# Optimization experiments

Hardware: AMD Instinct MI355X
Metric: run time of the kernel (lower is better)

## Reference

```python
import jax, jax.numpy as jnp
import numpy as np

WS = 7  # window_size
HEADS = 12
HEAD_DIM = 32
HIDDEN = 384
INNER = HEADS * HEAD_DIM


def _relative_position_index(ws):
    coords = np.stack(np.meshgrid(np.arange(ws), np.arange(ws), indexing='ij'))  # (2, ws, ws)
    flat = coords.reshape(2, -1)  # (2, ws*ws)
    rel = flat[:, :, None] - flat[:, None, :]  # (2, N, N)
    rel = rel.transpose(1, 2, 0).copy()
    rel[:, :, 0] += ws - 1
    rel[:, :, 1] += ws - 1
    rel[:, :, 0] *= 2 * ws - 1
    return rel.sum(-1)  # (N, N) int


def setup_inputs() -> dict:
    key = jax.random.key(0)
    k1, k2, k3, k4, k5 = jax.random.split(key, 5)
    x = jax.random.normal(k1, (32, 56, 56, HIDDEN), dtype=jnp.float32)
    w_qkv = jax.random.normal(k2, (HIDDEN, INNER * 3), dtype=jnp.float32) * (HIDDEN ** -0.5)
    w_out = jax.random.normal(k3, (INNER, HIDDEN), dtype=jnp.float32) * (INNER ** -0.5)
    b_out = jax.random.normal(k4, (HIDDEN,), dtype=jnp.float32) * 0.02
    bias_table = jax.random.normal(k5, ((2 * WS - 1) * (2 * WS - 1), HEADS), dtype=jnp.float32) * 0.02
    return {"x": x, "w_qkv": w_qkv, "w_out": w_out, "b_out": b_out, "bias_table": bias_table}


def _window_attention(x, w_qkv, w_out, b_out, bias_table):
    b, n_h, n_w, _ = x.shape
    ws, h, d = WS, HEADS, HEAD_DIM
    nw_h, nw_w = n_h // ws, n_w // ws
    N = ws * ws

    qkv = x @ w_qkv  # (b, n_h, n_w, 3*inner)
    q, k, v = jnp.split(qkv, 3, axis=-1)

    def to_windows(t):
        # (b, n_h, n_w, h*d) -> (b, h, nw_h*nw_w, ws*ws, d)
        t = t.reshape(b, nw_h, ws, nw_w, ws, h, d)
        t = t.transpose(0, 5, 1, 3, 2, 4, 6)
        return t.reshape(b, h, nw_h * nw_w, N, d)

    q, k, v = map(to_windows, (q, k, v))
    scale = d ** -0.5
    dots = jnp.einsum('bhwid,bhwjd->bhwij', q, k) * scale
    attn = jax.nn.softmax(dots, axis=-1)

    rel_idx = jnp.asarray(_relative_position_index(ws))  # (N, N)
    bias = bias_table[rel_idx.reshape(-1)].reshape(N, N, h)  # gather
    bias = bias.transpose(2, 0, 1)  # (h, N, N)
    # NOTE: faithful to source — bias added AFTER softmax
    attn = attn + bias[None, :, None, :, :]

    out = jnp.einsum('bhwij,bhwjd->bhwid', attn, v)  # (b, h, nw, N, d)
    out = out.reshape(b, h, nw_h, nw_w, ws, ws, d)
    out = out.transpose(0, 2, 4, 3, 5, 1, 6).reshape(b, n_h, n_w, h * d)
    return out @ w_out + b_out


def reference(x, w_qkv, w_out, b_out, bias_table):
    return _window_attention(x, w_qkv, w_out, b_out, bias_table)
```

## Files before the change

### kernel.cpp

```cpp
#include <hip/hip_runtime.h>
#include <hip/hip_bf16.h>
#include <cstdint>

#define TOK 100352
#define HID 384
#define NQKV 1152
#define NHEADS 12
#define HDIM 32

typedef __attribute__((ext_vector_type(8))) short bhalf8;
typedef __attribute__((ext_vector_type(4))) float f32x4;

__device__ __forceinline__ ushort f2bf(float f) {
  uint32_t u = __float_as_uint(f);
  return (ushort)((u + 0x7FFFu + ((u >> 16) & 1u)) >> 16);
}

__device__ __forceinline__ void gload_lds16(const ushort* g, ushort* l) {
  __builtin_amdgcn_global_load_lds(
      (const __attribute__((address_space(1))) unsigned int*)g,
      (__attribute__((address_space(3))) unsigned int*)l, 16, 0, 0);
}

__device__ __forceinline__ uint32_t cvtpk(float a, float b) {
  uint32_t r;
  asm("v_cvt_pk_bf16_f32 %0, %1, %2" : "=v"(r) : "v"(a), "v"(b));
  return r;
}

__global__ __launch_bounds__(256)
void cvt_bf16(const float* __restrict__ in, ushort* __restrict__ out, const int n8) {
  const int i = blockIdx.x * 256 + threadIdx.x;
  if (i >= n8) return;
  const float4 f0 = ((const float4*)in)[(size_t)i * 2];
  const float4 f1 = ((const float4*)in)[(size_t)i * 2 + 1];
  bhalf8 v;
  v[0] = (short)f2bf(f0.x); v[1] = (short)f2bf(f0.y);
  v[2] = (short)f2bf(f0.z); v[3] = (short)f2bf(f0.w);
  v[4] = (short)f2bf(f1.x); v[5] = (short)f2bf(f1.y);
  v[6] = (short)f2bf(f1.z); v[7] = (short)f2bf(f1.w);
  ((bhalf8*)out)[i] = v;
}

__global__ __launch_bounds__(256)
void transpose_cvt(const float* __restrict__ in, ushort* __restrict__ out,
                   const int R, const int C) {
  const int i = blockIdx.x * 256 + threadIdx.x;
  if (i >= R * C) return;
  const int r = i % R, c = i / R;
  out[i] = f2bf(in[(size_t)r * C + c]);
}

__global__ __launch_bounds__(256)
void expand_bias_pad(const float* __restrict__ bt, float* __restrict__ bx) {
  const int i = blockIdx.x * 256 + threadIdx.x;
  if (i >= NHEADS * 49 * 64) return;
  const int head = i / (49 * 64);
  const int rem = i % (49 * 64);
  const int q = rem / 64, k = rem % 64;
  float v = 0.f;
  if (k < 49) {
    const int idx = (q / 7 - k / 7 + 6) * 13 + (q % 7 - k % 7 + 6);
    v = bt[idx * NHEADS + head];
  }
  bx[i] = v;
}

template<bool OUT_F32_BIAS>
__global__ __launch_bounds__(256)
void gemm_bt(const ushort* __restrict__ A, const ushort* __restrict__ Bt,
             const float* __restrict__ bias, void* __restrict__ Cp,
             const int N, const int K, const int nbx, const int row_ofs)
{
  __shared__ ushort As[128 * 64];
  __shared__ ushort Bs[128 * 64];

  const int tid = threadIdx.x;
  const int lane = tid & 63;
  const int wave = tid >> 6;
  const int wm = wave >> 1, wn = wave & 1;
  const int l15 = lane & 15, l16 = lane >> 4;

  int bid = blockIdx.x;
  const int nwg = gridDim.x;
  if ((nwg & 7) == 0) bid = (bid & 7) * (nwg >> 3) + (bid >> 3);
  const int row0 = (bid / nbx) * 128 + row_ofs;
  const int col0 = (bid % nbx) * 128;

  f32x4 acc[4][4] = {};

  for (int ko = 0; ko < K; ko += 64) {
    if (ko) __syncthreads();
    #pragma unroll
    for (int it = 0; it < 4; ++it) {
      const int chunk = it * 4 + wave;
      const int idx = chunk * 64 + lane;
      const int m = idx >> 3;
      const int k8 = (((idx & 7) ^ (m & 7)) * 8);
      gload_lds16(A + (size_t)(row0 + m) * K + ko + k8, &As[chunk * 512]);
      gload_lds16(Bt + (size_t)(col0 + m) * K + ko + k8, &Bs[chunk * 512]);
    }
    __syncthreads();
    #pragma unroll
    for (int kk = 0; kk < 64; kk += 32) {
      bhalf8 af[4], bfr[4];
      #pragma unroll
      for (int f = 0; f < 4; ++f) {
        const int ra = wm * 64 + f * 16 + l15;
        const int rb = wn * 64 + f * 16 + l15;
        const int kb = (kk + l16 * 8) * 2;
        af[f]  = *(const bhalf8*)((const char*)As + ra * 128 + (kb ^ ((ra & 7) << 4)));
        bfr[f] = *(const bhalf8*)((const char*)Bs + rb * 128 + (kb ^ ((rb & 7) << 4)));
      }
      #pragma unroll
      for (int fm = 0; fm < 4; ++fm)
        #pragma unroll
        for (int fn = 0; fn < 4; ++fn)
          acc[fm][fn] = __builtin_amdgcn_mfma_f32_16x16x32_bf16(af[fm], bfr[fn], acc[fm][fn], 0, 0, 0);
    }
  }

  #pragma unroll
  for (int fm = 0; fm < 4; ++fm) {
    const int rb = row0 + wm * 64 + fm * 16 + l16 * 4;
    #pragma unroll
    for (int fn = 0; fn < 4; ++fn) {
      const int cc = col0 + wn * 64 + fn * 16 + l15;
      const float badd = OUT_F32_BIAS ? bias[cc] : 0.f;
      #pragma unroll
      for (int i = 0; i < 4; ++i) {
        const float vv = acc[fm][fn][i] + badd;
        if (OUT_F32_BIAS) ((float*)Cp)[(size_t)(rb + i) * N + cc] = vv;
        else ((ushort*)Cp)[(size_t)(rb + i) * N + cc] = f2bf(vv);
      }
    }
  }
}

__global__ __launch_bounds__(256)
void win_attn4(const ushort* __restrict__ qkv, const float* __restrict__ biasx,
               ushort* __restrict__ attn_out)
{
  __shared__ ushort VtAll[4][32 * 64];
  __shared__ ushort PsAll[4][64 * 64];

  const int tid = threadIdx.x;
  const int lane = tid & 63, wave = tid >> 6;
  const int l15 = lane & 15, l16 = lane >> 4;
  const int gid = blockIdx.x * 4 + wave;
  const int head = gid % NHEADS;
  const int win = gid / NHEADS;
  const int b = win >> 6, wi = (win >> 3) & 7, wj = win & 7;
  char* Vt = (char*)VtAll[wave];
  char* Ps = (char*)PsAll[wave];

  const int base_row = b * 3136 + wi * 7 * 56 + wj * 7;

  #pragma unroll
  for (int it = 0; it < 4; ++it) {
    const int t = lane;
    const int d0 = it * 8;
    bhalf8 v = {0, 0, 0, 0, 0, 0, 0, 0};
    if (t < 49) {
      const size_t off = (size_t)(base_row + (t / 7) * 56 + (t % 7)) * NQKV
                         + 768 + head * HDIM + d0;
      v = *(const bhalf8*)(qkv + off);
    }
    #pragma unroll
    for (int j = 0; j < 8; ++j) {
      const int d = d0 + j;
      const int byteoff = ((d * 64 + t) * 2) ^ ((d & 7) << 4);
      *(ushort*)(Vt + byteoff) = (ushort)v[j];
    }
  }

  bhalf8 qf[4], kf[4];
  #pragma unroll
  for (int f = 0; f < 4; ++f) {
    const int r = f * 16 + l15;
    const int rr = r < 49 ? r : 48;
    const size_t off = (size_t)(base_row + (rr / 7) * 56 + (rr % 7)) * NQKV
                       + head * HDIM + l16 * 8;
    qf[f] = *(const bhalf8*)(qkv + off);
    kf[f] = *(const bhalf8*)(qkv + off + 384);
  }

  const f32x4 fz = {};
  f32x4 s[4][4];
  #pragma unroll
  for (int fm = 0; fm < 4; ++fm)
    #pragma unroll
    for (int fn = 0; fn < 4; ++fn)
      s[fm][fn] = __builtin_amdgcn_mfma_f32_16x16x32_bf16(kf[fm], qf[fn], fz, 0, 0, 0);

  const float scale = 0.17677669529663687f;
  const float* bq = biasx + (size_t)head * (49 * 64);

  #pragma unroll
  for (int fn = 0; fn < 4; ++fn) {
    const int q = fn * 16 + l15;
    const int xr = (q & 7) << 4;
    char* prow = Ps + q * 128;
    if (fn == 3 && l15 != 0) {
      #pragma unroll
      for (int fm = 0; fm < 4; ++fm) {
        const int b0 = (fm * 16 + l16 * 4) * 2;
        *(uint32_t*)(prow + (b0 ^ xr)) = 0u;
        *(uint32_t*)(prow + (b0 ^ xr) + 4) = 0u;
      }
    } else {
      float e[4][4];
      float local = 0.f;
      #pragma unroll
      for (int fm = 0; fm < 3; ++fm)
        #pragma unroll
        for (int i = 0; i < 4; ++i) {
          e[fm][i] = __expf(s[fm][fn][i] * scale);
          local += e[fm][i];
        }
      e[3][0] = e[3][1] = e[3][2] = e[3][3] = 0.f;
      if (l16 == 0) {
        e[3][0] = __expf(s[3][fn][0] * scale);
        local += e[3][0];
      }
      float sum = local + __shfl_xor(local, 16);
      sum += __shfl_xor(sum, 32);
      const float inv = __builtin_amdgcn_rcpf(sum);
      const float* b4p = bq + q * 64;
      #pragma unroll
      for (int fm = 0; fm < 4; ++fm) {
        const int k0 = fm * 16 + l16 * 4;
        const float4 b4 = *(const float4*)(b4p + k0);
        const uint32_t w0 = cvtpk(fmaf(e[fm][0], inv, b4.x),
                                  fmaf(e[fm][1], inv, b4.y));
        const uint32_t w1 = cvtpk(fmaf(e[fm][2], inv, b4.z),
                                  fmaf(e[fm][3], inv, b4.w));
        const int b0 = (k0 * 2) ^ xr;
        *(uint32_t*)(prow + b0) = w0;
        *(uint32_t*)(prow + b0 + 4) = w1;
      }
    }
  }

  f32x4 o[4][2] = {};
  #pragma unroll
  for (int kk = 0; kk < 64; kk += 32) {
    bhalf8 pf[4], vf[2];
    #pragma unroll
    for (int f = 0; f < 4; ++f) {
      const int r = f * 16 + l15;
      pf[f] = *(const bhalf8*)(Ps + (((r * 64 + kk + l16 * 8) * 2) ^ ((r & 7) << 4)));
    }
    #pragma unroll
    for (int f = 0; f < 2; ++f) {
      const int d = f * 16 + l15;
      vf[f] = *(const bhalf8*)(Vt + (((d * 64 + kk + l16 * 8) * 2) ^ ((d & 7) << 4)));
    }
    #pragma unroll
    for (int fm = 0; fm < 4; ++fm)
      #pragma unroll
      for (int fn = 0; fn < 2; ++fn)
        o[fm][fn] = __builtin_amdgcn_mfma_f32_16x16x32_bf16(pf[fm], vf[fn], o[fm][fn], 0, 0, 0);
  }

  #pragma unroll
  for (int fm = 0; fm < 4; ++fm) {
    #pragma unroll
    for (int i = 0; i < 4; ++i) {
      const int r = fm * 16 + l16 * 4 + i;
      if (r < 49) {
        const int grow = base_row + (r / 7) * 56 + (r % 7);
        #pragma unroll
        for (int fn = 0; fn < 2; ++fn) {
          const int d = fn * 16 + l15;
          attn_out[(size_t)grow * HID + head * HDIM + d] = f2bf(o[fm][fn][i]);
        }
      }
    }
  }
}

extern "C" void kernel_launch(void* const* d_in, const int* in_sizes, int n_in,
                              void* d_out, int out_size, void* d_ws, size_t ws_size,
                              hipStream_t stream) {
  const float* x          = (const float*)d_in[0];
  const float* w_qkv      = (const float*)d_in[1];
  const float* w_out      = (const float*)d_in[2];
  const float* b_out      = (const float*)d_in[3];
  const float* bias_table = (const float*)d_in[4];
  float* out = (float*)d_out;

  ushort* xb     = (ushort*)d_ws;
  ushort* qkv    = xb + (size_t)TOK * HID;
  ushort* wqkvT  = qkv + (size_t)TOK * NQKV;
  ushort* woutT  = wqkvT + (size_t)NQKV * HID;
  float*  biasx  = (float*)(woutT + (size_t)HID * HID);
  ushort* attn_o = xb;

  {
    const int n8 = TOK * HID / 8;
    cvt_bf16<<<dim3((n8 + 255) / 256), dim3(256), 0, stream>>>(x, xb, n8);
    transpose_cvt<<<dim3(HID * NQKV / 256), dim3(256), 0, stream>>>(w_qkv, wqkvT, HID, NQKV);
    transpose_cvt<<<dim3(HID * HID / 256), dim3(256), 0, stream>>>(w_out, woutT, HID, HID);
    expand_bias_pad<<<dim3((NHEADS * 49 * 64 + 255) / 256), dim3(256), 0, stream>>>(
        bias_table, biasx);
  }

  const int halfM = TOK / 2;
  gemm_bt<false><<<dim3((NQKV / 128) * (halfM / 128)), dim3(256), 0, stream>>>(
      xb, wqkvT, nullptr, qkv, NQKV, HID, NQKV / 128, 0);
  gemm_bt<false><<<dim3((NQKV / 128) * (halfM / 128)), dim3(256), 0, stream>>>(
      xb, wqkvT, nullptr, qkv, NQKV, HID, NQKV / 128, halfM);

  win_attn4<<<dim3(2048 * NHEADS / 4), dim3(256), 0, stream>>>(qkv, biasx, attn_o);

  gemm_bt<true><<<dim3((HID / 128) * (TOK / 128)), dim3(256), 0, stream>>>(
      attn_o, woutT, b_out, out, HID, HID, HID / 128, 0);
}
```

Before: 344.5 us.

## Scatter QKV GEMM output into per-window, per-head contiguous layout

The QKV GEMM epilogue now writes each element directly into a window-major layout where every (window, head) owns contiguous Q, K and V slices of 49x32 bf16. The attention kernel can then read Q/K/V with simple contiguous offsets instead of strided gathers across image rows. The GEMM kernels are also specialized with compile-time N/K. The cost is a scattered 2-byte store pattern in the GEMM epilogue, with more index arithmetic per element and possibly poorly coalesced writes.

```diff
diff --git a/kernel.cpp b/kernel.cpp
--- a/kernel.cpp
+++ b/kernel.cpp
@@ -7,6 +7,7 @@
 #define NQKV 1152
 #define NHEADS 12
 #define HDIM 32
+#define WSLICE 1568
 
 typedef __attribute__((ext_vector_type(8))) short bhalf8;
 typedef __attribute__((ext_vector_type(4))) float f32x4;
@@ -66,11 +67,9 @@
   bx[i] = v;
 }
 
-template<bool OUT_F32_BIAS>
-__global__ __launch_bounds__(256)
-void gemm_bt(const ushort* __restrict__ A, const ushort* __restrict__ Bt,
-             const float* __restrict__ bias, void* __restrict__ Cp,
-             const int N, const int K, const int nbx, const int row_ofs)
+__global__ __launch_bounds__(256)
+void gemm_qkv_sc(const ushort* __restrict__ A, const ushort* __restrict__ Bt,
+                 ushort* __restrict__ qkvw, const int row_ofs)
 {
   __shared__ ushort As[128 * 64];
   __shared__ ushort Bs[128 * 64];
@@ -84,12 +83,12 @@
   int bid = blockIdx.x;
   const int nwg = gridDim.x;
   if ((nwg & 7) == 0) bid = (bid & 7) * (nwg >> 3) + (bid >> 3);
-  const int row0 = (bid / nbx) * 128 + row_ofs;
-  const int col0 = (bid % nbx) * 128;
+  const int row0 = (bid / 9) * 128 + row_ofs;
+  const int col0 = (bid % 9) * 128;
 
   f32x4 acc[4][4] = {};
 
-  for (int ko = 0; ko < K; ko += 64) {
+  for (int ko = 0; ko < HID; ko += 64) {
     if (ko) __syncthreads();
     #pragma unroll
     for (int it = 0; it < 4; ++it) {
@@ -97,8 +96,8 @@
       const int idx = chunk * 64 + lane;
       const int m = idx >> 3;
       const int k8 = (((idx & 7) ^ (m & 7)) * 8);
-      gload_lds16(A + (size_t)(row0 + m) * K + ko + k8, &As[chunk * 512]);
-      gload_lds16(Bt + (size_t)(col0 + m) * K + ko + k8, &Bs[chunk * 512]);
+      gload_lds16(A + (size_t)(row0 + m) * HID + ko + k8, &As[chunk * 512]);
+      gload_lds16(Bt + (size_t)(col0 + m) * HID + ko + k8, &Bs[chunk * 512]);
     }
     __syncthreads();
     #pragma unroll
@@ -122,23 +121,94 @@
 
   #pragma unroll
   for (int fm = 0; fm < 4; ++fm) {
+    #pragma unroll
+    for (int i = 0; i < 4; ++i) {
+      const int token = row0 + wm * 64 + fm * 16 + l16 * 4 + i;
+      const int bb = token / 3136, rem = token % 3136;
+      const int y = rem / 56, xx = rem % 56;
+      const int win = bb * 64 + (y / 7) * 8 + (xx / 7);
+      const int t = (y % 7) * 7 + (xx % 7);
+      ushort* tb = qkvw + (size_t)win * (NHEADS * 3 * WSLICE) + t * 32;
+      #pragma unroll
+      for (int fn = 0; fn < 4; ++fn) {
+        const int cc = col0 + wn * 64 + fn * 16 + l15;
+        const int sel = cc / 384;
+        const int hd = (cc % 384) >> 5;
+        const int d = cc & 31;
+        tb[(size_t)(hd * 3 + sel) * WSLICE + d] = f2bf(acc[fm][fn][i]);
+      }
+    }
+  }
+}
+
+__global__ __launch_bounds__(256)
+void gemm_out(const ushort* __restrict__ A, const ushort* __restrict__ Bt,
+              const float* __restrict__ bias, float* __restrict__ Cp)
+{
+  __shared__ ushort As[128 * 64];
+  __shared__ ushort Bs[128 * 64];
+
+  const int tid = threadIdx.x;
+  const int lane = tid & 63;
+  const int wave = tid >> 6;
+  const int wm = wave >> 1, wn = wave & 1;
+  const int l15 = lane & 15, l16 = lane >> 4;
+
+  int bid = blockIdx.x;
+  const int nwg = gridDim.x;
+  if ((nwg & 7) == 0) bid = (bid & 7) * (nwg >> 3) + (bid >> 3);
+  const int row0 = (bid / 3) * 128;
+  const int col0 = (bid % 3) * 128;
+
+  f32x4 acc[4][4] = {};
+
+  for (int ko = 0; ko < HID; ko += 64) {
+    if (ko) __syncthreads();
+    #pragma unroll
+    for (int it = 0; it < 4; ++it) {
+      const int chunk = it * 4 + wave;
+      const int idx = chunk * 64 + lane;
+      const int m = idx >> 3;
+      const int k8 = (((idx & 7) ^ (m & 7)) * 8);
+      gload_lds16(A + (size_t)(row0 + m) * HID + ko + k8, &As[chunk * 512]);
+      gload_lds16(Bt + (size_t)(col0 + m) * HID + ko + k8, &Bs[chunk * 512]);
+    }
+    __syncthreads();
+    #pragma unroll
+    for (int kk = 0; kk < 64; kk += 32) {
+      bhalf8 af[4], bfr[4];
+      #pragma unroll
+      for (int f = 0; f < 4; ++f) {
+        const int ra = wm * 64 + f * 16 + l15;
+        const int rb = wn * 64 + f * 16 + l15;
+        const int kb = (kk + l16 * 8) * 2;
+        af[f]  = *(const bhalf8*)((const char*)As + ra * 128 + (kb ^ ((ra & 7) << 4)));
+        bfr[f] = *(const bhalf8*)((const char*)Bs + rb * 128 + (kb ^ ((rb & 7) << 4)));
+      }
+      #pragma unroll
+      for (int fm = 0; fm < 4; ++fm)
+        #pragma unroll
+        for (int fn = 0; fn < 4; ++fn)
+          acc[fm][fn] = __builtin_amdgcn_mfma_f32_16x16x32_bf16(af[fm], bfr[fn], acc[fm][fn], 0, 0, 0);
+    }
+  }
+
+  #pragma unroll
+  for (int fm = 0; fm < 4; ++fm) {
     const int rb = row0 + wm * 64 + fm * 16 + l16 * 4;
     #pragma unroll
     for (int fn = 0; fn < 4; ++fn) {
       const int cc = col0 + wn * 64 + fn * 16 + l15;
-      const float badd = OUT_F32_BIAS ? bias[cc] : 0.f;
-      #pragma unroll
-      for (int i = 0; i < 4; ++i) {
-        const float vv = acc[fm][fn][i] + badd;
-        if (OUT_F32_BIAS) ((float*)Cp)[(size_t)(rb + i) * N + cc] = vv;
-        else ((ushort*)Cp)[(size_t)(rb + i) * N + cc] = f2bf(vv);
-      }
-    }
-  }
-}
-
-__global__ __launch_bounds__(256)
-void win_attn4(const ushort* __restrict__ qkv, const float* __restrict__ biasx,
+      const float badd = bias[cc];
+      #pragma unroll
+      for (int i = 0; i < 4; ++i)
+        Cp[(size_t)(rb + i) * HID + cc] = acc[fm][fn][i] + badd;
+    }
+  }
+}
+
+__global__ __launch_bounds__(256)
+void win_attn7(const ushort* __restrict__ qkvw, const float* __restrict__ biasx,
                ushort* __restrict__ attn_out)
 {
   __shared__ ushort VtAll[4][32 * 64];
@@ -154,6 +224,9 @@
   char* Vt = (char*)VtAll[wave];
   char* Ps = (char*)PsAll[wave];
 
+  const ushort* qb = qkvw + ((size_t)win * NHEADS + head) * (3 * WSLICE);
+  const ushort* kb = qb + WSLICE;
+  const ushort* vb = qb + 2 * WSLICE;
   const int base_row = b * 3136 + wi * 7 * 56 + wj * 7;
 
   #pragma unroll
@@ -161,11 +234,7 @@
     const int t = lane;
     const int d0 = it * 8;
     bhalf8 v = {0, 0, 0, 0, 0, 0, 0, 0};
-    if (t < 49) {
-      const size_t off = (size_t)(base_row + (t / 7) * 56 + (t % 7)) * NQKV
-                         + 768 + head * HDIM + d0;
-      v = *(const bhalf8*)(qkv + off);
-    }
+    if (t < 49) v = *(const bhalf8*)(vb + t * 32 + d0);
     #pragma unroll
     for (int j = 0; j < 8; ++j) {
       const int d = d0 + j;
@@ -179,10 +248,8 @@
   for (int f = 0; f < 4; ++f) {
     const int r = f * 16 + l15;
     const int rr = r < 49 ? r : 48;
-    const size_t off = (size_t)(base_row + (rr / 7) * 56 + (rr % 7)) * NQKV
-                       + head * HDIM + l16 * 8;
-    qf[f] = *(const bhalf8*)(qkv + off);
-    kf[f] = *(const bhalf8*)(qkv + off + 384);
+    qf[f] = *(const bhalf8*)(qb + rr * 32 + l16 * 8);
+    kf[f] = *(const bhalf8*)(kb + rr * 32 + l16 * 8);
   }
 
   const f32x4 fz = {};
@@ -291,8 +358,8 @@
   float* out = (float*)d_out;
 
   ushort* xb     = (ushort*)d_ws;
-  ushort* qkv    = xb + (size_t)TOK * HID;
-  ushort* wqkvT  = qkv + (size_t)TOK * NQKV;
+  ushort* qkvw   = xb + (size_t)TOK * HID;
+  ushort* wqkvT  = qkvw + (size_t)24576 * 3 * WSLICE;
   ushort* woutT  = wqkvT + (size_t)NQKV * HID;
   float*  biasx  = (float*)(woutT + (size_t)HID * HID);
   ushort* attn_o = xb;
@@ -307,13 +374,10 @@
   }
 
   const int halfM = TOK / 2;
-  gemm_bt<false><<<dim3((NQKV / 128) * (halfM / 128)), dim3(256), 0, stream>>>(
-      xb, wqkvT, nullptr, qkv, NQKV, HID, NQKV / 128, 0);
-  gemm_bt<false><<<dim3((NQKV / 128) * (halfM / 128)), dim3(256), 0, stream>>>(
-      xb, wqkvT, nullptr, qkv, NQKV, HID, NQKV / 128, halfM);
-
-  win_attn4<<<dim3(2048 * NHEADS / 4), dim3(256), 0, stream>>>(qkv, biasx, attn_o);
-
-  gemm_bt<true><<<dim3((HID / 128) * (TOK / 128)), dim3(256), 0, stream>>>(
-      attn_o, woutT, b_out, out, HID, HID, HID / 128, 0);
-}
+  gemm_qkv_sc<<<dim3(9 * (halfM / 128)), dim3(256), 0, stream>>>(xb, wqkvT, qkvw, 0);
+  gemm_qkv_sc<<<dim3(9 * (halfM / 128)), dim3(256), 0, stream>>>(xb, wqkvT, qkvw, halfM);
+
+  win_attn7<<<dim3(2048 * NHEADS / 4), dim3(256), 0, stream>>>(qkvw, biasx, attn_o);
+
+  gemm_out<<<dim3(3 * (TOK / 128)), dim3(256), 0, stream>>>(attn_o, woutT, b_out, out);
+}
```

New measurement: 349.7 us. No clear change (+1.5%).
